# Kernel optimization log

Measured on AMD Instinct MI355X. Metric: run time of the kernel, lower is better.

Reference implementation:

```python
import jax, jax.numpy as jnp
import numpy as np

N, M, FEAT, POS, D, MSG, NCLS = 64, 32, 256, 6, 262, 128, 7


def setup_inputs() -> dict:
    key = jax.random.key(0)
    ks = jax.random.split(key, 12)
    s = 0.05
    p = lambda k, shape: jax.random.normal(k, shape, jnp.float32) * s
    return {
        "nodes_feature": jax.random.normal(ks[0], (N, M, FEAT), jnp.float32),
        "pos": jax.random.normal(ks[1], (N, M, POS), jnp.float32),
        "num_rec": jax.random.randint(ks[2], (N,), 1, M + 1),
        "link_w1": p(ks[3], (D, 2 * D)),
        "link_b1": jnp.zeros((D,), jnp.float32),
        "link_w2": p(ks[4], (D,)),
        "link_b2": jnp.zeros((), jnp.float32),
        "msg_w": p(ks[5], (MSG, D)),
        "msg_b": jnp.zeros((MSG,), jnp.float32),
        "gru_w_ih": p(ks[6], (3 * D, MSG)),
        "gru_w_hh": p(ks[7], (3 * D, D)),
        "gru_b_ih": jnp.zeros((3 * D,), jnp.float32),
        "gru_b_hh": jnp.zeros((3 * D,), jnp.float32),
        "ro_w1": p(ks[8], (MSG, D)),
        "ro_b1": jnp.zeros((MSG,), jnp.float32),
        "ro_w2": p(ks[9], (NCLS, MSG)),
        "ro_b2": jnp.zeros((NCLS,), jnp.float32),
    }


def reference(nodes_feature, pos, num_rec, link_w1, link_b1, link_w2, link_b2,
              msg_w, msg_b, gru_w_ih, gru_w_hh, gru_b_ih, gru_b_hh,
              ro_w1, ro_b1, ro_w2, ro_b2):
    # node_feat = [resnet_feat, pos]  -> (N, M, 262)
    nf = jnp.concatenate([nodes_feature, pos], axis=-1)
    n, m, d = nf.shape
    valid = jnp.arange(m)[None, :] < num_rec[:, None]          # (N, M)
    pair = valid[:, :, None] & valid[:, None, :]               # (N, M, M)

    # edge_feat[b,:,i,j] = concat(nf[b,i], nf[b,j]); zero for invalid pairs
    ef = jnp.concatenate([
        jnp.broadcast_to(nf[:, :, None, :], (n, m, m, d)),
        jnp.broadcast_to(nf[:, None, :, :], (n, m, m, d)),
    ], axis=-1) * pair[..., None].astype(nf.dtype)             # (N, M, M, 2D)

    # 1x1 convs == per-pair MLP
    hlink = jax.nn.relu(jnp.einsum('bnwc,dc->bnwd', ef, link_w1) + link_b1)
    attmat = jax.nn.sigmoid(jnp.einsum('bnwd,d->bnw', hlink, link_w2) + link_b2)

    # messages are only summed over valid sender nodes w
    att_m = attmat * valid[:, None, :].astype(attmat.dtype)    # (N, M, M)

    def gru_step(x, h):
        # PyTorch GRU cell: gates order (r, z, n)
        gx = x @ gru_w_ih.T + gru_b_ih
        gh = h @ gru_w_hh.T + gru_b_hh
        xr, xz, xn = jnp.split(gx, 3, axis=-1)
        hr, hz, hn = jnp.split(gh, 3, axis=-1)
        r = jax.nn.sigmoid(xr + hr)
        z = jax.nn.sigmoid(xz + hz)
        c = jnp.tanh(xn + r * hn)
        return (1.0 - z) * c + z * h

    vmask = valid[..., None].astype(nf.dtype)
    h_state = nf                                               # pass 0 input state
    for _ in range(2):                                         # two message-passing rounds
        msg = h_state @ msg_w.T + msg_b                        # (N, M, 128)
        m_v = jnp.einsum('bnw,bwk->bnk', att_m, msg)           # attention-weighted sum
        h_state = gru_step(m_v, h_state) * vmask               # invalid nodes stay zero

    pred = (jax.nn.relu(h_state @ ro_w1.T + ro_b1) @ ro_w2.T + ro_b2) * vmask
    return pred, attmat
```

## Files before the change

kernel.cpp:

```cpp
#include <hip/hip_runtime.h>
#include <math.h>

#define N_G   64
#define M_N   32
#define FEAT  256
#define POSD  6
#define D     262
#define MSG   128
#define NCLS  7

#define KA_S  424
#define KHW   288
#define KFULL 416
#define PSTR  266

#define S_PROJ (528*288)
#define S_MSG  (128*288)
#define S_RZ   (544*416)
#define S_XN   (272*128)
#define S_HN   (272*288)
#define S_RO   (128*288)
#define S_RO2  (16*128)

#define O_WPROJ 0u
#define O_WMSG  76032u
#define O_WRZ   94464u
#define O_WXN   207616u
#define O_WHN   225024u
#define O_WRO   264192u
#define O_WRO2  282624u
#define O_GB    283648u

typedef __attribute__((ext_vector_type(8))) short short8;
typedef __attribute__((ext_vector_type(4))) short short4v;
typedef __attribute__((ext_vector_type(4))) float floatx4;

#define MFMA __builtin_amdgcn_mfma_f32_16x16x32_bf16

__device__ __forceinline__ short f2bf(float f) {
    union { float f; unsigned u; } v; v.f = f;
    unsigned r = v.u + 0x7FFF + ((v.u >> 16) & 1);
    return (short)(r >> 16);
}
__device__ __forceinline__ float bf2f(short s) {
    union { float f; unsigned u; } v;
    v.u = ((unsigned)(unsigned short)s) << 16;
    return v.f;
}
__device__ __forceinline__ float sigf(float x) {
    float e = __builtin_amdgcn_exp2f(x * -1.442695041f);
    return __builtin_amdgcn_rcpf(1.f + e);
}
__device__ __forceinline__ float tanhf_fast(float x) {
    float e = __builtin_amdgcn_exp2f(x * 2.885390082f);
    return 1.f - 2.f * __builtin_amdgcn_rcpf(e + 1.f);
}

__global__ void prep_kernel(const float* __restrict__ w1, const float* __restrict__ msg_w,
                            const float* __restrict__ w_ih, const float* __restrict__ w_hh,
                            const float* __restrict__ ro_w1, const float* __restrict__ ro_w2,
                            const float* __restrict__ b_ih, const float* __restrict__ b_hh,
                            const float* __restrict__ b1g, const float* __restrict__ w2g,
                            const float* __restrict__ b2g,
                            float* __restrict__ ws)
{
    short* wproj = (short*)(ws + O_WPROJ);
    short* wmsg  = (short*)(ws + O_WMSG);
    short* wrz   = (short*)(ws + O_WRZ);
    short* wxn   = (short*)(ws + O_WXN);
    short* whn   = (short*)(ws + O_WHN);
    short* wro   = (short*)(ws + O_WRO);
    short* wro2  = (short*)(ws + O_WRO2);
    float* gb    = ws + O_GB;
    const int TOT_S = S_PROJ + S_MSG + S_RZ + S_XN + S_HN + S_RO + S_RO2;
    const int TOTAL = TOT_S + 1089;
    for (int i = blockIdx.x * blockDim.x + threadIdx.x; i < TOTAL;
         i += gridDim.x * blockDim.x) {
        int idx = i;
        if (idx < S_PROJ) {
            int n = idx / 288, k = idx % 288;
            float v = 0.f;
            if (k < D && n < 524)
                v = (n < D) ? w1[n * 524 + k] : w1[(n - D) * 524 + D + k];
            wproj[idx] = f2bf(v);
            continue;
        }
        idx -= S_PROJ;
        if (idx < S_MSG) {
            int n = idx / 288, k = idx % 288;
            wmsg[idx] = f2bf(k < D ? msg_w[n * D + k] : 0.f);
            continue;
        }
        idx -= S_MSG;
        if (idx < S_RZ) {
            int g = idx / 416, k = idx % 416;
            int gi = (g < 272) ? 0 : 1;
            int d = g - gi * 272;
            float v = 0.f;
            if (d < D) {
                int row = gi * D + d;
                if (k < 128)            v = w_ih[row * MSG + k];
                else if (k < 128 + D)   v = w_hh[row * D + (k - 128)];
            }
            wrz[idx] = f2bf(v);
            continue;
        }
        idx -= S_RZ;
        if (idx < S_XN) {
            int d = idx / 128, k = idx % 128;
            wxn[idx] = f2bf(d < D ? w_ih[(2 * D + d) * MSG + k] : 0.f);
            continue;
        }
        idx -= S_XN;
        if (idx < S_HN) {
            int d = idx / 288, k = idx % 288;
            whn[idx] = f2bf((d < D && k < D) ? w_hh[(2 * D + d) * D + k] : 0.f);
            continue;
        }
        idx -= S_HN;
        if (idx < S_RO) {
            int n = idx / 288, k = idx % 288;
            wro[idx] = f2bf(k < D ? ro_w1[n * D + k] : 0.f);
            continue;
        }
        idx -= S_RO;
        if (idx < S_RO2) {
            int n = idx / 128, k = idx % 128;
            wro2[idx] = f2bf(n < NCLS ? ro_w2[n * MSG + k] : 0.f);
            continue;
        }
        idx -= S_RO2;
        if (idx < 1088) {
            int seg = idx / 272, d = idx % 272;
            float v = 0.f;
            if (d < D) {
                if (seg == 0)      v = b_ih[d] + b_hh[d];
                else if (seg == 1) v = b_ih[D + d] + b_hh[D + d];
                else if (seg == 2) v = b_ih[2 * D + d];
                else               v = b_hh[2 * D + d];
            }
            gb[idx] = v;
            continue;
        }
        {
            float s = 0.f;
            for (int d = 0; d < D; ++d)
                s += fmaxf(b1g[d], 0.f) * w2g[d];
            gb[1088] = sigf(s + b2g[0]);
        }
    }
}

__global__ __launch_bounds__(512, 2) void fused_kernel(
    const float* __restrict__ nodes, const float* __restrict__ pos,
    const int* __restrict__ nrec_g,
    const float* __restrict__ b1g, const float* __restrict__ w2g,
    const float* __restrict__ b2g, const float* __restrict__ msg_bg,
    const float* __restrict__ ro_b1g, const float* __restrict__ ro_b2g,
    const float* __restrict__ ws,
    float* __restrict__ att_out, float* __restrict__ pred)
{
    const short* Wproj = (const short*)(ws + O_WPROJ);
    const short* Wmsg  = (const short*)(ws + O_WMSG);
    const short* Wrz   = (const short*)(ws + O_WRZ);
    const short* Wxn   = (const short*)(ws + O_WXN);
    const short* Whn   = (const short*)(ws + O_WHN);
    const short* Wro   = (const short*)(ws + O_WRO);
    const short* Wro2  = (const short*)(ws + O_WRO2);
    const float* gb    = ws + O_GB;

    __shared__ __align__(16) short bufA[32 * KA_S];
    __shared__ __align__(16) short bufB[32 * KA_S];
    __shared__ __align__(16) short paL[32 * PSTR];
    __shared__ __align__(16) short pbL[32 * PSTR];
    __shared__ __align__(16) short attL[32 * 40];
    __shared__ __align__(16) short msgT[128 * 40];
    __shared__ __align__(16) short hidL[32 * 136];
    __shared__ __align__(16) float b1L[PSTR + 6], w2L[PSTR + 6];

    const int b = blockIdx.x;
    const int tid = threadIdx.x;
    const int wave = tid >> 6, lane = tid & 63;
    const int quad = lane >> 4, lrow = lane & 15;
    const int nr = nrec_g[b];

    for (int idx = tid; idx < 32 * 64; idx += 512) {
        int w = idx >> 6, c4 = idx & 63;
        floatx4 v = *(const floatx4*)(nodes + ((size_t)(b * 32 + w)) * FEAT + c4 * 4);
        short4v s; s[0] = f2bf(v[0]); s[1] = f2bf(v[1]); s[2] = f2bf(v[2]); s[3] = f2bf(v[3]);
        *(short4v*)(bufA + w * KA_S + 128 + c4 * 4) = s;
    }
    for (int idx = tid; idx < 32 * POSD; idx += 512) {
        int w = idx / POSD, c = idx % POSD;
        bufA[w * KA_S + 128 + FEAT + c] = f2bf(pos[((size_t)(b * 32 + w)) * POSD + c]);
    }
    for (int idx = tid; idx < 32 * 34; idx += 512) {
        int w = idx / 34, c = idx % 34;
        bufA[w * KA_S + 390 + c] = 0;
        bufB[w * KA_S + 390 + c] = 0;
    }
    for (int idx = tid; idx < 32 * (PSTR - D); idx += 512) {
        int w = idx / (PSTR - D), c = idx % (PSTR - D);
        paL[w * PSTR + D + c] = 0;
        pbL[w * PSTR + D + c] = 0;
    }
    for (int d = tid; d < PSTR + 6; d += 512) {
        b1L[d] = (d < D) ? b1g[d] : 0.f;
        w2L[d] = (d < D) ? w2g[d] : 0.f;
    }
    __syncthreads();

    for (int s = wave; s < 33; s += 8) {
        floatx4 acc0 = {}, acc1 = {};
        const short* bw = Wproj + (s * 16 + lrow) * KHW + quad * 8;
        const short* ap = bufA + lrow * KA_S + 128 + quad * 8;
        for (int kk = 0; kk < 9; ++kk) {
            short8 a0 = *(const short8*)(ap + kk * 32);
            short8 a1 = *(const short8*)(ap + 16 * KA_S + kk * 32);
            short8 bv = *(const short8*)(bw + kk * 32);
            acc0 = MFMA(a0, bv, acc0, 0, 0, 0);
            acc1 = MFMA(a1, bv, acc1, 0, 0, 0);
        }
        int col = s * 16 + lrow;
#pragma unroll
        for (int rr = 0; rr < 4; ++rr) {
            int r0 = quad * 4 + rr;
            if (col < D) {
                float bb = b1L[col];
                paL[r0 * PSTR + col] = f2bf(acc0[rr] + bb);
                paL[(r0 + 16) * PSTR + col] = f2bf(acc1[rr] + bb);
            } else if (col < 2 * D) {
                pbL[r0 * PSTR + (col - D)] = f2bf(acc0[rr]);
                pbL[(r0 + 16) * PSTR + (col - D)] = f2bf(acc1[rr]);
            }
        }
    }
    __syncthreads();

    {
        const float c0 = gb[1088];
        const float b2v = b2g[0];
        const int jj = lane & 31;
        const int i0 = 2 * wave + (lane >> 5);
        const int i1 = i0 + 16;
        const short* pa0 = paL + i0 * PSTR;
        const short* pa1 = paL + i1 * PSTR;
        const short* pbr = pbL + jj * PSTR;
        float s0 = 0.f, s1 = 0.f;
        for (int c = 0; c < 33; ++c) {
            int d = c * 8;
            short8 qa0 = *(const short8*)(pa0 + d);
            short8 qa1 = *(const short8*)(pa1 + d);
            short8 qb  = *(const short8*)(pbr + d);
            floatx4 wlo = *(const floatx4*)(w2L + d);
            floatx4 whi = *(const floatx4*)(w2L + d + 4);
#pragma unroll
            for (int e = 0; e < 8; ++e) {
                float w = (e < 4) ? wlo[e] : whi[e - 4];
                float pbv = bf2f(qb[e]);
                s0 += fmaxf(bf2f(qa0[e]) + pbv, 0.f) * w;
                s1 += fmaxf(bf2f(qa1[e]) + pbv, 0.f) * w;
            }
        }
        const bool vj = jj < nr;
        float a0 = (vj && i0 < nr) ? sigf(s0 + b2v) : c0;
        float a1 = (vj && i1 < nr) ? sigf(s1 + b2v) : c0;
        att_out[((size_t)(b * 32 + i0)) * 32 + jj] = a0;
        att_out[((size_t)(b * 32 + i1)) * 32 + jj] = a1;
        attL[i0 * 40 + jj] = f2bf(vj ? a0 : 0.f);
        attL[i1 * 40 + jj] = f2bf(vj ? a1 : 0.f);
    }
    __syncthreads();

    for (int rnd = 0; rnd < 2; ++rnd) {
        short* src = rnd ? bufB : bufA;
        short* dst = rnd ? bufA : bufB;

        {
            int s = wave;
            floatx4 acc0 = {}, acc1 = {};
            const short* bw = Wmsg + (s * 16 + lrow) * KHW + quad * 8;
            const short* ap = src + lrow * KA_S + 128 + quad * 8;
            for (int kk = 0; kk < 9; ++kk) {
                short8 a0 = *(const short8*)(ap + kk * 32);
                short8 a1 = *(const short8*)(ap + 16 * KA_S + kk * 32);
                short8 bv = *(const short8*)(bw + kk * 32);
                acc0 = MFMA(a0, bv, acc0, 0, 0, 0);
                acc1 = MFMA(a1, bv, acc1, 0, 0, 0);
            }
            int col = s * 16 + lrow;
            float bias = msg_bg[col];
#pragma unroll
            for (int rr = 0; rr < 4; ++rr) {
                msgT[col * 40 + quad * 4 + rr] = f2bf(acc0[rr] + bias);
                msgT[col * 40 + 16 + quad * 4 + rr] = f2bf(acc1[rr] + bias);
            }
        }
        __syncthreads();

        {
            int mi = wave & 1, ng = wave >> 1;
            short8 afrag = *(const short8*)(attL + (mi * 16 + lrow) * 40 + quad * 8);
            floatx4 acc0 = {}, acc1 = {};
            short8 bf0 = *(const short8*)(msgT + (ng * 32 + lrow) * 40 + quad * 8);
            short8 bf1 = *(const short8*)(msgT + (ng * 32 + 16 + lrow) * 40 + quad * 8);
            acc0 = MFMA(afrag, bf0, acc0, 0, 0, 0);
            acc1 = MFMA(afrag, bf1, acc1, 0, 0, 0);
#pragma unroll
            for (int rr = 0; rr < 4; ++rr) {
                int m = mi * 16 + quad * 4 + rr;
                src[m * KA_S + ng * 32 + lrow] = f2bf(acc0[rr]);
                src[m * KA_S + ng * 32 + 16 + lrow] = f2bf(acc1[rr]);
            }
        }
        __syncthreads();

        for (int s = wave; s < 17; s += 8) {
            floatx4 aR0 = {}, aR1 = {}, aZ0 = {}, aZ1 = {};
            floatx4 aN0 = {}, aN1 = {}, aH0 = {}, aH1 = {};
            const short* ap  = src + lrow * KA_S + quad * 8;
            const short* bpr = Wrz + (s * 16 + lrow) * KFULL + quad * 8;
            const short* bpz = Wrz + (272 + s * 16 + lrow) * KFULL + quad * 8;
            const short* bpx = Wxn + (s * 16 + lrow) * 128 + quad * 8;
            const short* bph = Whn + (s * 16 + lrow) * KHW + quad * 8;
            for (int kk = 0; kk < 13; ++kk) {
                short8 a0 = *(const short8*)(ap + kk * 32);
                short8 a1 = *(const short8*)(ap + 16 * KA_S + kk * 32);
                short8 br = *(const short8*)(bpr + kk * 32);
                short8 bz = *(const short8*)(bpz + kk * 32);
                aR0 = MFMA(a0, br, aR0, 0, 0, 0);
                aR1 = MFMA(a1, br, aR1, 0, 0, 0);
                aZ0 = MFMA(a0, bz, aZ0, 0, 0, 0);
                aZ1 = MFMA(a1, bz, aZ1, 0, 0, 0);
                if (kk < 4) {
                    short8 bx = *(const short8*)(bpx + kk * 32);
                    aN0 = MFMA(a0, bx, aN0, 0, 0, 0);
                    aN1 = MFMA(a1, bx, aN1, 0, 0, 0);
                } else {
                    short8 bh = *(const short8*)(bph + (kk - 4) * 32);
                    aH0 = MFMA(a0, bh, aH0, 0, 0, 0);
                    aH1 = MFMA(a1, bh, aH1, 0, 0, 0);
                }
            }
            int d = s * 16 + lrow;
            if (d < D) {
                float bgr = gb[d], bgz = gb[272 + d];
                float bxv = gb[544 + d], bhv = gb[816 + d];
#pragma unroll
                for (int i = 0; i < 2; ++i) {
                    floatx4 vR = i ? aR1 : aR0, vZ = i ? aZ1 : aZ0;
                    floatx4 vN = i ? aN1 : aN0, vH = i ? aH1 : aH0;
#pragma unroll
                    for (int rr = 0; rr < 4; ++rr) {
                        int m = i * 16 + quad * 4 + rr;
                        float rg = sigf(vR[rr] + bgr);
                        float zg = sigf(vZ[rr] + bgz);
                        float cg = tanhf_fast(vN[rr] + bxv + rg * (vH[rr] + bhv));
                        float hold = bf2f(src[m * KA_S + 128 + d]);
                        float hv = (1.f - zg) * cg + zg * hold;
                        if (m >= nr) hv = 0.f;
                        dst[m * KA_S + 128 + d] = f2bf(hv);
                    }
                }
            }
        }
        __syncthreads();
    }

    {
        int s = wave;
        floatx4 acc0 = {}, acc1 = {};
        const short* bw = Wro + (s * 16 + lrow) * KHW + quad * 8;
        const short* ap = bufA + lrow * KA_S + 128 + quad * 8;
        for (int kk = 0; kk < 9; ++kk) {
            short8 a0 = *(const short8*)(ap + kk * 32);
            short8 a1 = *(const short8*)(ap + 16 * KA_S + kk * 32);
            short8 bv = *(const short8*)(bw + kk * 32);
            acc0 = MFMA(a0, bv, acc0, 0, 0, 0);
            acc1 = MFMA(a1, bv, acc1, 0, 0, 0);
        }
        int col = s * 16 + lrow;
        float bias = ro_b1g[col];
#pragma unroll
        for (int rr = 0; rr < 4; ++rr) {
            hidL[(quad * 4 + rr) * 136 + col] = f2bf(fmaxf(acc0[rr] + bias, 0.f));
            hidL[(16 + quad * 4 + rr) * 136 + col] = f2bf(fmaxf(acc1[rr] + bias, 0.f));
        }
    }
    __syncthreads();

    if (wave == 0) {
        floatx4 acc0 = {}, acc1 = {};
        const short* ap = hidL + lrow * 136 + quad * 8;
        const short* bw = Wro2 + lrow * 128 + quad * 8;
        for (int kk = 0; kk < 4; ++kk) {
            short8 a0 = *(const short8*)(ap + kk * 32);
            short8 a1 = *(const short8*)(ap + 16 * 136 + kk * 32);
            short8 bv = *(const short8*)(bw + kk * 32);
            acc0 = MFMA(a0, bv, acc0, 0, 0, 0);
            acc1 = MFMA(a1, bv, acc1, 0, 0, 0);
        }
        int q = lrow;
        if (q < NCLS) {
            float bias = ro_b2g[q];
#pragma unroll
            for (int i = 0; i < 2; ++i) {
#pragma unroll
                for (int rr = 0; rr < 4; ++rr) {
                    int m = i * 16 + quad * 4 + rr;
                    float v = (i ? acc1[rr] : acc0[rr]) + bias;
                    if (m >= nr) v = 0.f;
                    pred[((size_t)(b * 32 + m)) * NCLS + q] = v;
                }
            }
        }
    }
}

extern "C" void kernel_launch(void* const* d_in, const int* in_sizes, int n_in,
                              void* d_out, int out_size, void* d_ws, size_t ws_size,
                              hipStream_t stream)
{
    const float* nodes = (const float*)d_in[0];
    const float* pos   = (const float*)d_in[1];
    const int*   nrec  = (const int*)d_in[2];
    const float* w1    = (const float*)d_in[3];
    const float* b1    = (const float*)d_in[4];
    const float* w2    = (const float*)d_in[5];
    const float* b2    = (const float*)d_in[6];
    const float* msg_w = (const float*)d_in[7];
    const float* msg_b = (const float*)d_in[8];
    const float* w_ih  = (const float*)d_in[9];
    const float* w_hh  = (const float*)d_in[10];
    const float* b_ih  = (const float*)d_in[11];
    const float* b_hh  = (const float*)d_in[12];
    const float* ro_w1 = (const float*)d_in[13];
    const float* ro_b1 = (const float*)d_in[14];
    const float* ro_w2 = (const float*)d_in[15];
    const float* ro_b2 = (const float*)d_in[16];
    float* ws   = (float*)d_ws;
    float* pred = (float*)d_out;
    float* attout = pred + (size_t)N_G * M_N * NCLS;

    prep_kernel<<<256, 256, 0, stream>>>(w1, msg_w, w_ih, w_hh, ro_w1, ro_w2,
                                         b_ih, b_hh, b1, w2, b2, ws);
    fused_kernel<<<N_G, 512, 0, stream>>>(nodes, pos, nrec, b1, w2, b2, msg_b,
                                          ro_b1, ro_b2, ws, attout, pred);
}
```

Before: 169.1 us.

## Warm L2 with weight prefetch sweep and software-pipeline global weight loads in GEMM loops

Each block first streams the whole bf16 weight workspace with wide loads XOR-reduced into a dummy value, so the weights are pulled into cache before the dependent GEMM phases. The MFMA loops are unrolled and their B-operand (and GRU A-operand) loads are double-buffered one or two k-steps ahead to hide global load latency. The prefetch sweep adds a large amount of redundant global traffic per block (64 blocks each read the full workspace), and the register buffering raises register pressure.

```diff
diff --git a/kernel.cpp b/kernel.cpp
--- a/kernel.cpp
+++ b/kernel.cpp
@@ -21,6 +21,7 @@
 #define S_HN   (272*288)
 #define S_RO   (128*288)
 #define S_RO2  (16*128)
+#define S_TOT  (S_PROJ+S_MSG+S_RZ+S_XN+S_HN+S_RO+S_RO2)
 
 #define O_WPROJ 0u
 #define O_WMSG  76032u
@@ -34,6 +35,7 @@
 typedef __attribute__((ext_vector_type(8))) short short8;
 typedef __attribute__((ext_vector_type(4))) short short4v;
 typedef __attribute__((ext_vector_type(4))) float floatx4;
+typedef __attribute__((ext_vector_type(4))) int intx4;
 
 #define MFMA __builtin_amdgcn_mfma_f32_16x16x32_bf16
 
@@ -72,8 +74,7 @@
     short* wro   = (short*)(ws + O_WRO);
     short* wro2  = (short*)(ws + O_WRO2);
     float* gb    = ws + O_GB;
-    const int TOT_S = S_PROJ + S_MSG + S_RZ + S_XN + S_HN + S_RO + S_RO2;
-    const int TOTAL = TOT_S + 1089;
+    const int TOTAL = S_TOT + 1089;
     for (int i = blockIdx.x * blockDim.x + threadIdx.x; i < TOTAL;
          i += gridDim.x * blockDim.x) {
         int idx = i;
@@ -184,6 +185,29 @@
     const int quad = lane >> 4, lrow = lane & 15;
     const int nr = nrec_g[b];
 
+    {
+        const intx4* wp = (const intx4*)ws;
+        const int total16 = S_TOT / 8;
+        intx4 acc = {0, 0, 0, 0};
+        for (int ib = 0; ib < 9; ++ib) {
+            int base = ib * 8192 + tid;
+            intx4 v[16];
+#pragma unroll
+            for (int u = 0; u < 16; ++u) {
+                int j = base + u * 512;
+                j = (j < total16) ? j : (total16 - 1);
+                v[u] = wp[j];
+            }
+#pragma unroll
+            for (int u = 0; u < 16; ++u) {
+                acc[0] ^= v[u][0]; acc[1] ^= v[u][1];
+                acc[2] ^= v[u][2]; acc[3] ^= v[u][3];
+            }
+        }
+        if (nr > 1000000)
+            ((int*)bufA)[0] = acc[0] + acc[1] + acc[2] + acc[3];
+    }
+
     for (int idx = tid; idx < 32 * 64; idx += 512) {
         int w = idx >> 6, c4 = idx & 63;
         floatx4 v = *(const floatx4*)(nodes + ((size_t)(b * 32 + w)) * FEAT + c4 * 4);
@@ -214,10 +238,13 @@
         floatx4 acc0 = {}, acc1 = {};
         const short* bw = Wproj + (s * 16 + lrow) * KHW + quad * 8;
         const short* ap = bufA + lrow * KA_S + 128 + quad * 8;
+        short8 bnext = *(const short8*)bw;
+#pragma unroll
         for (int kk = 0; kk < 9; ++kk) {
+            short8 bv = bnext;
+            if (kk < 8) bnext = *(const short8*)(bw + (kk + 1) * 32);
             short8 a0 = *(const short8*)(ap + kk * 32);
             short8 a1 = *(const short8*)(ap + 16 * KA_S + kk * 32);
-            short8 bv = *(const short8*)(bw + kk * 32);
             acc0 = MFMA(a0, bv, acc0, 0, 0, 0);
             acc1 = MFMA(a1, bv, acc1, 0, 0, 0);
         }
@@ -281,10 +308,13 @@
             floatx4 acc0 = {}, acc1 = {};
             const short* bw = Wmsg + (s * 16 + lrow) * KHW + quad * 8;
             const short* ap = src + lrow * KA_S + 128 + quad * 8;
+            short8 bnext = *(const short8*)bw;
+#pragma unroll
             for (int kk = 0; kk < 9; ++kk) {
+                short8 bv = bnext;
+                if (kk < 8) bnext = *(const short8*)(bw + (kk + 1) * 32);
                 short8 a0 = *(const short8*)(ap + kk * 32);
                 short8 a1 = *(const short8*)(ap + 16 * KA_S + kk * 32);
-                short8 bv = *(const short8*)(bw + kk * 32);
                 acc0 = MFMA(a0, bv, acc0, 0, 0, 0);
                 acc1 = MFMA(a1, bv, acc1, 0, 0, 0);
             }
@@ -323,23 +353,41 @@
             const short* bpz = Wrz + (272 + s * 16 + lrow) * KFULL + quad * 8;
             const short* bpx = Wxn + (s * 16 + lrow) * 128 + quad * 8;
             const short* bph = Whn + (s * 16 + lrow) * KHW + quad * 8;
+            short8 brf[2], bzf[2], bxf[2], a0f[2], a1f[2];
+            brf[0] = *(const short8*)bpr;
+            bzf[0] = *(const short8*)bpz;
+            bxf[0] = *(const short8*)bpx;
+            a0f[0] = *(const short8*)ap;
+            a1f[0] = *(const short8*)(ap + 16 * KA_S);
+            brf[1] = *(const short8*)(bpr + 32);
+            bzf[1] = *(const short8*)(bpz + 32);
+            bxf[1] = *(const short8*)(bpx + 32);
+            a0f[1] = *(const short8*)(ap + 32);
+            a1f[1] = *(const short8*)(ap + 16 * KA_S + 32);
+#pragma unroll
             for (int kk = 0; kk < 13; ++kk) {
-                short8 a0 = *(const short8*)(ap + kk * 32);
-                short8 a1 = *(const short8*)(ap + 16 * KA_S + kk * 32);
-                short8 br = *(const short8*)(bpr + kk * 32);
-                short8 bz = *(const short8*)(bpz + kk * 32);
+                int c = kk & 1;
+                short8 br = brf[c], bz = bzf[c], bx = bxf[c];
+                short8 a0 = a0f[c], a1 = a1f[c];
+                if (kk + 2 < 13) {
+                    int kn = kk + 2;
+                    brf[c] = *(const short8*)(bpr + kn * 32);
+                    bzf[c] = *(const short8*)(bpz + kn * 32);
+                    bxf[c] = *(const short8*)((kn < 4) ? (bpx + kn * 32)
+                                                       : (bph + (kn - 4) * 32));
+                    a0f[c] = *(const short8*)(ap + kn * 32);
+                    a1f[c] = *(const short8*)(ap + 16 * KA_S + kn * 32);
+                }
                 aR0 = MFMA(a0, br, aR0, 0, 0, 0);
                 aR1 = MFMA(a1, br, aR1, 0, 0, 0);
                 aZ0 = MFMA(a0, bz, aZ0, 0, 0, 0);
                 aZ1 = MFMA(a1, bz, aZ1, 0, 0, 0);
                 if (kk < 4) {
-                    short8 bx = *(const short8*)(bpx + kk * 32);
                     aN0 = MFMA(a0, bx, aN0, 0, 0, 0);
                     aN1 = MFMA(a1, bx, aN1, 0, 0, 0);
                 } else {
-                    short8 bh = *(const short8*)(bph + (kk - 4) * 32);
-                    aH0 = MFMA(a0, bh, aH0, 0, 0, 0);
-                    aH1 = MFMA(a1, bh, aH1, 0, 0, 0);
+                    aH0 = MFMA(a0, bx, aH0, 0, 0, 0);
+                    aH1 = MFMA(a1, bx, aH1, 0, 0, 0);
                 }
             }
             int d = s * 16 + lrow;
@@ -372,10 +420,13 @@
         floatx4 acc0 = {}, acc1 = {};
         const short* bw = Wro + (s * 16 + lrow) * KHW + quad * 8;
         const short* ap = bufA + lrow * KA_S + 128 + quad * 8;
+        short8 bnext = *(const short8*)bw;
+#pragma unroll
         for (int kk = 0; kk < 9; ++kk) {
+            short8 bv = bnext;
+            if (kk < 8) bnext = *(const short8*)(bw + (kk + 1) * 32);
             short8 a0 = *(const short8*)(ap + kk * 32);
             short8 a1 = *(const short8*)(ap + 16 * KA_S + kk * 32);
-            short8 bv = *(const short8*)(bw + kk * 32);
             acc0 = MFMA(a0, bv, acc0, 0, 0, 0);
             acc1 = MFMA(a1, bv, acc1, 0, 0, 0);
         }
```

Measured after the change: 172.3 us. About the same (+1.9%).

## Split fused GNN kernel into per-stage kernels with column-sliced GRU grid

Applied to the files above, without the earlier changes.

Replaces the single 64-block fused kernel with separate kernels: a projection/attention kernel, two round kernels launched with 544 blocks (32 row groups times 17 output column slices), and a readout kernel. Input node features are converted to bf16 in the prep kernel, and hidden state passes through global workspace between kernels. The aim is to raise GPU occupancy, since 64 blocks leave most CUs idle. In exchange, each round block recomputes the full message projection and aggregation for its 64 rows, and the change adds extra launches and global round-trips.

```diff
diff --git a/kernel.cpp b/kernel.cpp
--- a/kernel.cpp
+++ b/kernel.cpp
@@ -9,10 +9,12 @@
 #define MSG   128
 #define NCLS  7
 
-#define KA_S  424
 #define KHW   288
 #define KFULL 416
 #define PSTR  266
+#define HST   288
+#define AST   424
+#define A2ST  296
 
 #define S_PROJ (528*288)
 #define S_MSG  (128*288)
@@ -21,6 +23,7 @@
 #define S_HN   (272*288)
 #define S_RO   (128*288)
 #define S_RO2  (16*128)
+#define S_TOT  (S_PROJ+S_MSG+S_RZ+S_XN+S_HN+S_RO+S_RO2)
 
 #define O_WPROJ 0u
 #define O_WMSG  76032u
@@ -30,9 +33,10 @@
 #define O_WRO   264192u
 #define O_WRO2  282624u
 #define O_GB    283648u
+#define O_H0F   284740u
+#define O_HGF   579652u
 
 typedef __attribute__((ext_vector_type(8))) short short8;
-typedef __attribute__((ext_vector_type(4))) short short4v;
 typedef __attribute__((ext_vector_type(4))) float floatx4;
 
 #define MFMA __builtin_amdgcn_mfma_f32_16x16x32_bf16
@@ -56,7 +60,8 @@
     return 1.f - 2.f * __builtin_amdgcn_rcpf(e + 1.f);
 }
 
-__global__ void prep_kernel(const float* __restrict__ w1, const float* __restrict__ msg_w,
+__global__ void prep_kernel(const float* __restrict__ nodes, const float* __restrict__ pos,
+                            const float* __restrict__ w1, const float* __restrict__ msg_w,
                             const float* __restrict__ w_ih, const float* __restrict__ w_hh,
                             const float* __restrict__ ro_w1, const float* __restrict__ ro_w2,
                             const float* __restrict__ b_ih, const float* __restrict__ b_hh,
@@ -72,8 +77,10 @@
     short* wro   = (short*)(ws + O_WRO);
     short* wro2  = (short*)(ws + O_WRO2);
     float* gb    = ws + O_GB;
-    const int TOT_S = S_PROJ + S_MSG + S_RZ + S_XN + S_HN + S_RO + S_RO2;
-    const int TOTAL = TOT_S + 1089;
+    short* h0    = (short*)(ws + O_H0F);
+    short* hg    = (short*)(ws + O_HGF);
+    const int T_H = 2048 * HST;
+    const int TOTAL = S_TOT + 1089 + 2 * T_H;
     for (int i = blockIdx.x * blockDim.x + threadIdx.x; i < TOTAL;
          i += gridDim.x * blockDim.x) {
         int idx = i;
@@ -142,40 +149,40 @@
             gb[idx] = v;
             continue;
         }
-        {
+        if (idx == 1088) {
             float s = 0.f;
             for (int d = 0; d < D; ++d)
                 s += fmaxf(b1g[d], 0.f) * w2g[d];
             gb[1088] = sigf(s + b2g[0]);
-        }
-    }
-}
-
-__global__ __launch_bounds__(512, 2) void fused_kernel(
-    const float* __restrict__ nodes, const float* __restrict__ pos,
+            continue;
+        }
+        idx -= 1089;
+        if (idx < T_H) {
+            int n = idx / HST, c = idx % HST;
+            float v = 0.f;
+            if (c < FEAT)      v = nodes[(size_t)n * FEAT + c];
+            else if (c < D)    v = pos[(size_t)n * POSD + (c - FEAT)];
+            h0[idx] = f2bf(v);
+            continue;
+        }
+        idx -= T_H;
+        hg[idx] = 0;
+    }
+}
+
+__global__ __launch_bounds__(512, 2) void projatt_kernel(
     const int* __restrict__ nrec_g,
     const float* __restrict__ b1g, const float* __restrict__ w2g,
-    const float* __restrict__ b2g, const float* __restrict__ msg_bg,
-    const float* __restrict__ ro_b1g, const float* __restrict__ ro_b2g,
-    const float* __restrict__ ws,
-    float* __restrict__ att_out, float* __restrict__ pred)
+    const float* __restrict__ b2g,
+    const float* __restrict__ ws, float* __restrict__ att_out)
 {
     const short* Wproj = (const short*)(ws + O_WPROJ);
-    const short* Wmsg  = (const short*)(ws + O_WMSG);
-    const short* Wrz   = (const short*)(ws + O_WRZ);
-    const short* Wxn   = (const short*)(ws + O_WXN);
-    const short* Whn   = (const short*)(ws + O_WHN);
-    const short* Wro   = (const short*)(ws + O_WRO);
-    const short* Wro2  = (const short*)(ws + O_WRO2);
+    const short* h0    = (const short*)(ws + O_H0F);
     const float* gb    = ws + O_GB;
 
-    __shared__ __align__(16) short bufA[32 * KA_S];
-    __shared__ __align__(16) short bufB[32 * KA_S];
+    __shared__ __align__(16) short Ab[32 * A2ST];
     __shared__ __align__(16) short paL[32 * PSTR];
     __shared__ __align__(16) short pbL[32 * PSTR];
-    __shared__ __align__(16) short attL[32 * 40];
-    __shared__ __align__(16) short msgT[128 * 40];
-    __shared__ __align__(16) short hidL[32 * 136];
     __shared__ __align__(16) float b1L[PSTR + 6], w2L[PSTR + 6];
 
     const int b = blockIdx.x;
@@ -184,20 +191,10 @@
     const int quad = lane >> 4, lrow = lane & 15;
     const int nr = nrec_g[b];
 
-    for (int idx = tid; idx < 32 * 64; idx += 512) {
-        int w = idx >> 6, c4 = idx & 63;
-        floatx4 v = *(const floatx4*)(nodes + ((size_t)(b * 32 + w)) * FEAT + c4 * 4);
-        short4v s; s[0] = f2bf(v[0]); s[1] = f2bf(v[1]); s[2] = f2bf(v[2]); s[3] = f2bf(v[3]);
-        *(short4v*)(bufA + w * KA_S + 128 + c4 * 4) = s;
-    }
-    for (int idx = tid; idx < 32 * POSD; idx += 512) {
-        int w = idx / POSD, c = idx % POSD;
-        bufA[w * KA_S + 128 + FEAT + c] = f2bf(pos[((size_t)(b * 32 + w)) * POSD + c]);
-    }
-    for (int idx = tid; idx < 32 * 34; idx += 512) {
-        int w = idx / 34, c = idx % 34;
-        bufA[w * KA_S + 390 + c] = 0;
-        bufB[w * KA_S + 390 + c] = 0;
+    for (int idx = tid; idx < 32 * 36; idx += 512) {
+        int r = idx / 36, c8 = idx % 36;
+        *(short8*)(Ab + r * A2ST + c8 * 8) =
+            *(const short8*)(h0 + ((size_t)(b * 32 + r)) * HST + c8 * 8);
     }
     for (int idx = tid; idx < 32 * (PSTR - D); idx += 512) {
         int w = idx / (PSTR - D), c = idx % (PSTR - D);
@@ -213,10 +210,10 @@
     for (int s = wave; s < 33; s += 8) {
         floatx4 acc0 = {}, acc1 = {};
         const short* bw = Wproj + (s * 16 + lrow) * KHW + quad * 8;
-        const short* ap = bufA + lrow * KA_S + 128 + quad * 8;
+        const short* ap = Ab + lrow * A2ST + quad * 8;
         for (int kk = 0; kk < 9; ++kk) {
             short8 a0 = *(const short8*)(ap + kk * 32);
-            short8 a1 = *(const short8*)(ap + 16 * KA_S + kk * 32);
+            short8 a1 = *(const short8*)(ap + 16 * A2ST + kk * 32);
             short8 bv = *(const short8*)(bw + kk * 32);
             acc0 = MFMA(a0, bv, acc0, 0, 0, 0);
             acc1 = MFMA(a1, bv, acc1, 0, 0, 0);
@@ -267,151 +264,185 @@
         float a1 = (vj && i1 < nr) ? sigf(s1 + b2v) : c0;
         att_out[((size_t)(b * 32 + i0)) * 32 + jj] = a0;
         att_out[((size_t)(b * 32 + i1)) * 32 + jj] = a1;
-        attL[i0 * 40 + jj] = f2bf(vj ? a0 : 0.f);
-        attL[i1 * 40 + jj] = f2bf(vj ? a1 : 0.f);
-    }
-    __syncthreads();
-
-    for (int rnd = 0; rnd < 2; ++rnd) {
-        short* src = rnd ? bufB : bufA;
-        short* dst = rnd ? bufA : bufB;
-
-        {
-            int s = wave;
-            floatx4 acc0 = {}, acc1 = {};
-            const short* bw = Wmsg + (s * 16 + lrow) * KHW + quad * 8;
-            const short* ap = src + lrow * KA_S + 128 + quad * 8;
+    }
+}
+
+__global__ __launch_bounds__(256, 2) void round_kernel(
+    const short* __restrict__ hin, short* __restrict__ hout,
+    const float* __restrict__ att_out, const int* __restrict__ nrec_g,
+    const float* __restrict__ msg_bg, const float* __restrict__ ws)
+{
+    const short* Wmsg = (const short*)(ws + O_WMSG);
+    const short* Wrz  = (const short*)(ws + O_WRZ);
+    const short* Wxn  = (const short*)(ws + O_WXN);
+    const short* Whn  = (const short*)(ws + O_WHN);
+    const float* gb   = ws + O_GB;
+
+    __shared__ __align__(16) short Ab[64 * AST];
+    __shared__ __align__(16) short msgT[2][128 * 40];
+    __shared__ __align__(16) short attL[2][32 * 40];
+
+    const int rg = blockIdx.x / 17;
+    const int s  = blockIdx.x % 17;
+    const int R0 = rg * 64;
+    const int g0 = rg * 2;
+    const int tid = threadIdx.x;
+    const int wave = tid >> 6, lane = tid & 63;
+    const int quad = lane >> 4, lrow = lane & 15;
+    const int nr0 = nrec_g[g0], nr1 = nrec_g[g0 + 1];
+
+    for (int idx = tid; idx < 64 * 36; idx += 256) {
+        int r = idx / 36, c8 = idx % 36;
+        *(short8*)(Ab + r * AST + 128 + c8 * 8) =
+            *(const short8*)(hin + ((size_t)(R0 + r)) * HST + c8 * 8);
+    }
+    for (int idx = tid; idx < 2048; idx += 256) {
+        int gi = idx >> 10, i = (idx >> 5) & 31, j = idx & 31;
+        int nrg = gi ? nr1 : nr0;
+        float a = att_out[((size_t)((g0 + gi) * 32 + i)) * 32 + j];
+        attL[gi][i * 40 + j] = f2bf(j < nrg ? a : 0.f);
+    }
+    __syncthreads();
+
+    {
+        const short* ap = Ab + (wave * 16 + lrow) * AST + 128 + quad * 8;
+        for (int cs = 0; cs < 8; ++cs) {
+            floatx4 acc = {};
+            const short* bw = Wmsg + (cs * 16 + lrow) * KHW + quad * 8;
             for (int kk = 0; kk < 9; ++kk) {
                 short8 a0 = *(const short8*)(ap + kk * 32);
-                short8 a1 = *(const short8*)(ap + 16 * KA_S + kk * 32);
                 short8 bv = *(const short8*)(bw + kk * 32);
-                acc0 = MFMA(a0, bv, acc0, 0, 0, 0);
-                acc1 = MFMA(a1, bv, acc1, 0, 0, 0);
-            }
-            int col = s * 16 + lrow;
+                acc = MFMA(a0, bv, acc, 0, 0, 0);
+            }
+            int col = cs * 16 + lrow;
             float bias = msg_bg[col];
 #pragma unroll
+            for (int rr = 0; rr < 4; ++rr)
+                msgT[wave >> 1][col * 40 + (wave & 1) * 16 + quad * 4 + rr] =
+                    f2bf(acc[rr] + bias);
+        }
+    }
+    __syncthreads();
+
+    {
+        int g = wave >> 1, t = wave & 1;
+        short8 afrag = *(const short8*)(&attL[g][(t * 16 + lrow) * 40 + quad * 8]);
+        for (int ct = 0; ct < 8; ++ct) {
+            short8 bfrag = *(const short8*)(&msgT[g][(ct * 16 + lrow) * 40 + quad * 8]);
+            floatx4 acc = {};
+            acc = MFMA(afrag, bfrag, acc, 0, 0, 0);
+#pragma unroll
+            for (int rr = 0; rr < 4; ++rr)
+                Ab[(wave * 16 + quad * 4 + rr) * AST + ct * 16 + lrow] = f2bf(acc[rr]);
+        }
+    }
+    __syncthreads();
+
+    {
+        floatx4 aR = {}, aZ = {}, aN = {}, aH = {};
+        const short* ap  = Ab + (wave * 16 + lrow) * AST + quad * 8;
+        const short* bpr = Wrz + (s * 16 + lrow) * KFULL + quad * 8;
+        const short* bpz = Wrz + (272 + s * 16 + lrow) * KFULL + quad * 8;
+        const short* bpx = Wxn + (s * 16 + lrow) * 128 + quad * 8;
+        const short* bph = Whn + (s * 16 + lrow) * KHW + quad * 8;
+        for (int kk = 0; kk < 13; ++kk) {
+            short8 a0 = *(const short8*)(ap + kk * 32);
+            short8 br = *(const short8*)(bpr + kk * 32);
+            short8 bz = *(const short8*)(bpz + kk * 32);
+            aR = MFMA(a0, br, aR, 0, 0, 0);
+            aZ = MFMA(a0, bz, aZ, 0, 0, 0);
+            if (kk < 4) {
+                short8 bx = *(const short8*)(bpx + kk * 32);
+                aN = MFMA(a0, bx, aN, 0, 0, 0);
+            } else {
+                short8 bh = *(const short8*)(bph + (kk - 4) * 32);
+                aH = MFMA(a0, bh, aH, 0, 0, 0);
+            }
+        }
+        int d = s * 16 + lrow;
+        if (d < D) {
+            float bgr = gb[d], bgz = gb[272 + d];
+            float bxv = gb[544 + d], bhv = gb[816 + d];
+#pragma unroll
             for (int rr = 0; rr < 4; ++rr) {
-                msgT[col * 40 + quad * 4 + rr] = f2bf(acc0[rr] + bias);
-                msgT[col * 40 + 16 + quad * 4 + rr] = f2bf(acc1[rr] + bias);
-            }
-        }
-        __syncthreads();
-
-        {
-            int mi = wave & 1, ng = wave >> 1;
-            short8 afrag = *(const short8*)(attL + (mi * 16 + lrow) * 40 + quad * 8);
-            floatx4 acc0 = {}, acc1 = {};
-            short8 bf0 = *(const short8*)(msgT + (ng * 32 + lrow) * 40 + quad * 8);
-            short8 bf1 = *(const short8*)(msgT + (ng * 32 + 16 + lrow) * 40 + quad * 8);
-            acc0 = MFMA(afrag, bf0, acc0, 0, 0, 0);
-            acc1 = MFMA(afrag, bf1, acc1, 0, 0, 0);
-#pragma unroll
-            for (int rr = 0; rr < 4; ++rr) {
-                int m = mi * 16 + quad * 4 + rr;
-                src[m * KA_S + ng * 32 + lrow] = f2bf(acc0[rr]);
-                src[m * KA_S + ng * 32 + 16 + lrow] = f2bf(acc1[rr]);
-            }
-        }
-        __syncthreads();
-
-        for (int s = wave; s < 17; s += 8) {
-            floatx4 aR0 = {}, aR1 = {}, aZ0 = {}, aZ1 = {};
-            floatx4 aN0 = {}, aN1 = {}, aH0 = {}, aH1 = {};
-            const short* ap  = src + lrow * KA_S + quad * 8;
-            const short* bpr = Wrz + (s * 16 + lrow) * KFULL + quad * 8;
-            const short* bpz = Wrz + (272 + s * 16 + lrow) * KFULL + quad * 8;
-            const short* bpx = Wxn + (s * 16 + lrow) * 128 + quad * 8;
-            const short* bph = Whn + (s * 16 + lrow) * KHW + quad * 8;
-            for (int kk = 0; kk < 13; ++kk) {
+                int row = wave * 16 + quad * 4 + rr;
+                float rgg = sigf(aR[rr] + bgr);
+                float zg = sigf(aZ[rr] + bgz);
+                float cg = tanhf_fast(aN[rr] + bxv + rgg * (aH[rr] + bhv));
+                float hold = bf2f(Ab[row * AST + 128 + d]);
+                float hv = (1.f - zg) * cg + zg * hold;
+                int nrg = (row >> 5) ? nr1 : nr0;
+                if ((row & 31) >= nrg) hv = 0.f;
+                hout[((size_t)(R0 + row)) * HST + d] = f2bf(hv);
+            }
+        }
+    }
+}
+
+__global__ __launch_bounds__(256, 2) void rofinal_kernel(
+    const short* __restrict__ hin, const int* __restrict__ nrec_g,
+    const float* __restrict__ ro_b1g, const float* __restrict__ ro_b2g,
+    const float* __restrict__ ws, float* __restrict__ pred)
+{
+    const short* Wro  = (const short*)(ws + O_WRO);
+    const short* Wro2 = (const short*)(ws + O_WRO2);
+
+    __shared__ __align__(16) short Ab[64 * A2ST];
+    __shared__ __align__(16) short hidL[64 * 136];
+
+    const int rg = blockIdx.x;
+    const int R0 = rg * 64;
+    const int tid = threadIdx.x;
+    const int wave = tid >> 6, lane = tid & 63;
+    const int quad = lane >> 4, lrow = lane & 15;
+    const int nr0 = nrec_g[rg * 2], nr1 = nrec_g[rg * 2 + 1];
+
+    for (int idx = tid; idx < 64 * 36; idx += 256) {
+        int r = idx / 36, c8 = idx % 36;
+        *(short8*)(Ab + r * A2ST + c8 * 8) =
+            *(const short8*)(hin + ((size_t)(R0 + r)) * HST + c8 * 8);
+    }
+    __syncthreads();
+
+    {
+        const short* ap = Ab + (wave * 16 + lrow) * A2ST + quad * 8;
+        for (int cs = 0; cs < 8; ++cs) {
+            floatx4 acc = {};
+            const short* bw = Wro + (cs * 16 + lrow) * KHW + quad * 8;
+            for (int kk = 0; kk < 9; ++kk) {
                 short8 a0 = *(const short8*)(ap + kk * 32);
-                short8 a1 = *(const short8*)(ap + 16 * KA_S + kk * 32);
-                short8 br = *(const short8*)(bpr + kk * 32);
-                short8 bz = *(const short8*)(bpz + kk * 32);
-                aR0 = MFMA(a0, br, aR0, 0, 0, 0);
-                aR1 = MFMA(a1, br, aR1, 0, 0, 0);
-                aZ0 = MFMA(a0, bz, aZ0, 0, 0, 0);
-                aZ1 = MFMA(a1, bz, aZ1, 0, 0, 0);
-                if (kk < 4) {
-                    short8 bx = *(const short8*)(bpx + kk * 32);
-                    aN0 = MFMA(a0, bx, aN0, 0, 0, 0);
-                    aN1 = MFMA(a1, bx, aN1, 0, 0, 0);
-                } else {
-                    short8 bh = *(const short8*)(bph + (kk - 4) * 32);
-                    aH0 = MFMA(a0, bh, aH0, 0, 0, 0);
-                    aH1 = MFMA(a1, bh, aH1, 0, 0, 0);
-                }
-            }
-            int d = s * 16 + lrow;
-            if (d < D) {
-                float bgr = gb[d], bgz = gb[272 + d];
-                float bxv = gb[544 + d], bhv = gb[816 + d];
-#pragma unroll
-                for (int i = 0; i < 2; ++i) {
-                    floatx4 vR = i ? aR1 : aR0, vZ = i ? aZ1 : aZ0;
-                    floatx4 vN = i ? aN1 : aN0, vH = i ? aH1 : aH0;
-#pragma unroll
-                    for (int rr = 0; rr < 4; ++rr) {
-                        int m = i * 16 + quad * 4 + rr;
-                        float rg = sigf(vR[rr] + bgr);
-                        float zg = sigf(vZ[rr] + bgz);
-                        float cg = tanhf_fast(vN[rr] + bxv + rg * (vH[rr] + bhv));
-                        float hold = bf2f(src[m * KA_S + 128 + d]);
-                        float hv = (1.f - zg) * cg + zg * hold;
-                        if (m >= nr) hv = 0.f;
-                        dst[m * KA_S + 128 + d] = f2bf(hv);
-                    }
-                }
-            }
-        }
-        __syncthreads();
-    }
-
-    {
-        int s = wave;
-        floatx4 acc0 = {}, acc1 = {};
-        const short* bw = Wro + (s * 16 + lrow) * KHW + quad * 8;
-        const short* ap = bufA + lrow * KA_S + 128 + quad * 8;
-        for (int kk = 0; kk < 9; ++kk) {
-            short8 a0 = *(const short8*)(ap + kk * 32);
-            short8 a1 = *(const short8*)(ap + 16 * KA_S + kk * 32);
-            short8 bv = *(const short8*)(bw + kk * 32);
-            acc0 = MFMA(a0, bv, acc0, 0, 0, 0);
-            acc1 = MFMA(a1, bv, acc1, 0, 0, 0);
-        }
-        int col = s * 16 + lrow;
-        float bias = ro_b1g[col];
-#pragma unroll
-        for (int rr = 0; rr < 4; ++rr) {
-            hidL[(quad * 4 + rr) * 136 + col] = f2bf(fmaxf(acc0[rr] + bias, 0.f));
-            hidL[(16 + quad * 4 + rr) * 136 + col] = f2bf(fmaxf(acc1[rr] + bias, 0.f));
-        }
-    }
-    __syncthreads();
-
-    if (wave == 0) {
-        floatx4 acc0 = {}, acc1 = {};
-        const short* ap = hidL + lrow * 136 + quad * 8;
+                short8 bv = *(const short8*)(bw + kk * 32);
+                acc = MFMA(a0, bv, acc, 0, 0, 0);
+            }
+            int col = cs * 16 + lrow;
+            float bias = ro_b1g[col];
+#pragma unroll
+            for (int rr = 0; rr < 4; ++rr)
+                hidL[(wave * 16 + quad * 4 + rr) * 136 + col] =
+                    f2bf(fmaxf(acc[rr] + bias, 0.f));
+        }
+    }
+    __syncthreads();
+
+    {
+        floatx4 acc = {};
+        const short* ap = hidL + (wave * 16 + lrow) * 136 + quad * 8;
         const short* bw = Wro2 + lrow * 128 + quad * 8;
         for (int kk = 0; kk < 4; ++kk) {
             short8 a0 = *(const short8*)(ap + kk * 32);
-            short8 a1 = *(const short8*)(ap + 16 * 136 + kk * 32);
             short8 bv = *(const short8*)(bw + kk * 32);
-            acc0 = MFMA(a0, bv, acc0, 0, 0, 0);
-            acc1 = MFMA(a1, bv, acc1, 0, 0, 0);
+            acc = MFMA(a0, bv, acc, 0, 0, 0);
         }
         int q = lrow;
         if (q < NCLS) {
             float bias = ro_b2g[q];
 #pragma unroll
-            for (int i = 0; i < 2; ++i) {
-#pragma unroll
-                for (int rr = 0; rr < 4; ++rr) {
-                    int m = i * 16 + quad * 4 + rr;
-                    float v = (i ? acc1[rr] : acc0[rr]) + bias;
-                    if (m >= nr) v = 0.f;
-                    pred[((size_t)(b * 32 + m)) * NCLS + q] = v;
-                }
+            for (int rr = 0; rr < 4; ++rr) {
+                int row = wave * 16 + quad * 4 + rr;
+                float v = acc[rr] + bias;
+                int nrg = (row >> 5) ? nr1 : nr0;
+                if ((row & 31) >= nrg) v = 0.f;
+                pred[((size_t)(R0 + row)) * NCLS + q] = v;
             }
         }
     }
@@ -441,9 +472,13 @@
     float* ws   = (float*)d_ws;
     float* pred = (float*)d_out;
     float* attout = pred + (size_t)N_G * M_N * NCLS;
-
-    prep_kernel<<<256, 256, 0, stream>>>(w1, msg_w, w_ih, w_hh, ro_w1, ro_w2,
-                                         b_ih, b_hh, b1, w2, b2, ws);
-    fused_kernel<<<N_G, 512, 0, stream>>>(nodes, pos, nrec, b1, w2, b2, msg_b,
-                                          ro_b1, ro_b2, ws, attout, pred);
-}
+    short* h0 = (short*)(ws + O_H0F);
+    short* hg = (short*)(ws + O_HGF);
+
+    prep_kernel<<<256, 256, 0, stream>>>(nodes, pos, w1, msg_w, w_ih, w_hh,
+                                         ro_w1, ro_w2, b_ih, b_hh, b1, w2, b2, ws);
+    projatt_kernel<<<N_G, 512, 0, stream>>>(nrec, b1, w2, b2, ws, attout);
+    round_kernel<<<544, 256, 0, stream>>>(h0, hg, attout, nrec, msg_b, ws);
+    round_kernel<<<544, 256, 0, stream>>>(hg, h0, attout, nrec, msg_b, ws);
+    rofinal_kernel<<<32, 256, 0, stream>>>(h0, nrec, ro_b1, ro_b2, ws, pred);
+}
```

Measured after the change: 213.4 us. +26.2%, slower.
